# Kernel tuning notes

Measured on AMD Instinct MI355X. Metric: run time of the kernel, lower is better.

Reference implementation:

```python
import jax, jax.numpy as jnp
import numpy as np

B, C, H, W = 8, 256, 128, 128
KC, VC, HEADS = 256, 256, 8


def setup_inputs() -> dict:
    key = jax.random.key(0)
    ks = jax.random.split(key, 10)
    s = 0.05
    return {
        "x": jax.random.normal(ks[0], (B, C, H, W), jnp.float32),
        "Wk": jax.random.normal(ks[1], (KC, C), jnp.float32) * s,
        "bk": jax.random.normal(ks[2], (KC,), jnp.float32) * s,
        "Wq": jax.random.normal(ks[3], (KC, C), jnp.float32) * s,
        "bq": jax.random.normal(ks[4], (KC,), jnp.float32) * s,
        "Wv": jax.random.normal(ks[5], (VC, C), jnp.float32) * s,
        "bv": jax.random.normal(ks[6], (VC,), jnp.float32) * s,
        "Wr": jax.random.normal(ks[7], (C, VC), jnp.float32) * s,
        "br": jax.random.normal(ks[8], (C,), jnp.float32) * s,
        "head_count": HEADS,
    }


def reference(x, Wk, bk, Wq, bq, Wv, bv, Wr, br, head_count):
    n, c, h, w = x.shape
    hw = h * w
    xf = x.reshape(n, c, hw)  # [n, C, S]
    # 1x1 convs == per-pixel linear projections
    keys = jnp.einsum('kc,ncs->nks', Wk, xf) + bk[None, :, None]
    queries = jnp.einsum('kc,ncs->nks', Wq, xf) + bq[None, :, None]
    values = jnp.einsum('vc,ncs->nvs', Wv, xf) + bv[None, :, None]

    dk = Wk.shape[0] // head_count
    dv = Wv.shape[0] // head_count
    # split heads along channel dim (matches torch channel slicing)
    K = jax.nn.softmax(keys.reshape(n, head_count, dk, hw), axis=-1)   # softmax over spatial
    Q = jax.nn.softmax(queries.reshape(n, head_count, dk, hw), axis=2) # softmax over key dim
    V = values.reshape(n, head_count, dv, hw)

    # context = K @ V^T : [n, h, dk, dv]
    ctx = jnp.einsum('nhks,nhvs->nhkv', K, V)
    # attended = ctx^T @ Q : [n, h, dv, S]
    att = jnp.einsum('nhkv,nhks->nhvs', ctx, Q).reshape(n, head_count * dv, h, w)

    attention = jnp.einsum('ov,nvhw->nohw', Wr, att) + br[None, :, None, None]
    # attention map: per-head mean over key dim, then mean over heads
    attention_map = K.mean(axis=2).mean(axis=1).reshape(n, h, w)
    # torch returns the LAST head's context (loop variable after the loop)
    context_last = ctx[:, -1]
    return attention, context_last, attention_map
```

## Files before the change

kernel.cpp:

```cpp
#include <hip/hip_runtime.h>
#include <hip/hip_bf16.h>

typedef float f32x4 __attribute__((ext_vector_type(4)));
typedef short s16x8 __attribute__((ext_vector_type(8)));
typedef short s16x4 __attribute__((ext_vector_type(4)));
typedef __bf16 bf16x8 __attribute__((ext_vector_type(8)));
typedef unsigned short u16;

#define DEVI __device__ __forceinline__

static constexpr int    HW      = 16384;
static constexpr size_t BSTRIDE = (size_t)256 * HW;

static constexpr size_t oXBT   = 0;
static constexpr size_t oEK    = oXBT  + (size_t)8 * HW * 256 * 2;
static constexpr size_t oQT    = oEK   + (size_t)8 * 256 * HW * 2;
static constexpr size_t oVB    = oQT   + (size_t)8 * HW * 256 * 2;
static constexpr size_t oWK    = oVB   + (size_t)8 * 256 * HW * 2;
static constexpr size_t oBIAS  = oWK   + (size_t)768 * 256 * 2;
static constexpr size_t oISE   = oBIAS + 4096;
static constexpr size_t oPS    = oISE  + 8192;
static constexpr size_t oCTX   = oPS   + (size_t)256 * 2048 * 4;
static constexpr size_t oMB    = oCTX  + (size_t)64 * 1024 * 4;
static constexpr size_t oCPART = oMB   + (size_t)8 * 256 * 256 * 2;
static constexpr size_t oMPART = oCPART + (size_t)4096 * 1024 * 4;

DEVI float bf2f(short x) {
  unsigned u = ((unsigned)(unsigned short)x) << 16;
  return __builtin_bit_cast(float, u);
}
DEVI u16 f2bf(float x) { return __builtin_bit_cast(u16, (__bf16)x); }

DEVI void gld16(const void* g, void* l) {
  __builtin_amdgcn_global_load_lds(
      (__attribute__((address_space(1))) void*)(g),
      (__attribute__((address_space(3))) void*)(l), 16, 0, 0);
}

__global__ __launch_bounds__(256) void k_pt(
    const float* __restrict__ x,
    const float* __restrict__ Wk, const float* __restrict__ Wq, const float* __restrict__ Wv,
    const float* __restrict__ bk, const float* __restrict__ bq, const float* __restrict__ bv,
    u16* __restrict__ xbT, u16* __restrict__ Wkqv, float* __restrict__ bias)
{
  __shared__ u16 lds[64 * 256];
  const int t = threadIdx.x;
  const int tb = blockIdx.x;
  if (tb < 2048) {
    const int n = tb >> 8;
    const int s0 = (tb & 255) * 64;
    const float* src = x + ((size_t)n * 256 + t) * HW + s0;
    #pragma unroll
    for (int i = 0; i < 16; ++i) {
      f32x4 v = *(const f32x4*)(src + i * 4);
      #pragma unroll
      for (int j = 0; j < 4; ++j) lds[(i * 4 + j) * 256 + t] = f2bf(v[j]);
    }
    __syncthreads();
    s16x8* gp = (s16x8*)(xbT + (size_t)n * BSTRIDE + (size_t)s0 * 256);
    const s16x8* lp = (const s16x8*)lds;
    #pragma unroll
    for (int i = 0; i < 8; ++i) gp[t + i * 256] = lp[t + i * 256];
  } else {
    const int i = (tb - 2048) * 256 + t;
    for (int p = i; p < 768 * 256; p += 64 * 256) {
      float v = (p < 65536) ? Wk[p] : (p < 131072 ? Wq[p - 65536] : Wv[p - 131072]);
      Wkqv[p] = f2bf(v);
    }
    if (i < 768) bias[i] = (i < 256) ? bk[i] : (i < 512 ? bq[i - 256] : bv[i - 512]);
  }
}

#define GEMM_CORE(Ab, Bb)                                                                   \
  u16* Al = smem;                                                                           \
  u16* Bl = smem + 16384;                                                                   \
  auto STAGE = [&](int buf, int kt) {                                                       \
    const int k0 = kt * 64;                                                                 \
    _Pragma("unroll")                                                                       \
    for (int i = 0; i < 4; ++i) {                                                           \
      const int r_ = i * 32 + (t >> 3);                                                     \
      const int cs = (((t & 7) ^ (r_ & 7)) * 8);                                            \
      gld16((Ab) + (size_t)r_ * 256 + k0 + cs, Al + buf * 8192 + i * 2048 + t * 8);         \
      gld16((Bb) + (size_t)r_ * 256 + k0 + cs, Bl + buf * 8192 + i * 2048 + t * 8);         \
    }                                                                                       \
  };                                                                                        \
  f32x4 acc[4][4] = {};                                                                     \
  STAGE(0, 0); STAGE(1, 1);                                                                 \
  _Pragma("unroll")                                                                         \
  for (int kt = 0; kt < 4; ++kt) {                                                          \
    if (kt < 3) asm volatile("s_waitcnt vmcnt(8)" ::: "memory");                            \
    else        asm volatile("s_waitcnt vmcnt(0)" ::: "memory");                            \
    __builtin_amdgcn_s_barrier();                                                           \
    const int buf = kt & 1;                                                                 \
    _Pragma("unroll")                                                                       \
    for (int ks = 0; ks < 2; ++ks) {                                                        \
      bf16x8 af[4], bff[4];                                                                 \
      _Pragma("unroll")                                                                     \
      for (int g = 0; g < 4; ++g) {                                                         \
        const int mrow = wm + g * 16 + l15;                                                 \
        const int srow = wn + g * 16 + l15;                                                 \
        af[g]  = *(const bf16x8*)&Al[buf * 8192 + mrow * 64 + (((ks * 4 + l4) ^ (mrow & 7)) * 8)]; \
        bff[g] = *(const bf16x8*)&Bl[buf * 8192 + srow * 64 + (((ks * 4 + l4) ^ (srow & 7)) * 8)]; \
      }                                                                                     \
      __builtin_amdgcn_s_setprio(1);                                                        \
      _Pragma("unroll")                                                                     \
      for (int mg = 0; mg < 4; ++mg)                                                        \
        _Pragma("unroll")                                                                   \
        for (int ng = 0; ng < 4; ++ng)                                                      \
          acc[mg][ng] = __builtin_amdgcn_mfma_f32_16x16x32_bf16(af[mg], bff[ng], acc[mg][ng], 0, 0, 0); \
      __builtin_amdgcn_s_setprio(0);                                                        \
    }                                                                                       \
    asm volatile("s_waitcnt lgkmcnt(0)" ::: "memory");                                      \
    __builtin_amdgcn_s_barrier();                                                           \
    if (kt < 2) STAGE(buf, kt + 2);                                                         \
  }

__global__ __launch_bounds__(256, 2) void k_proj(
    const u16* __restrict__ W, const u16* __restrict__ xbT, const float* __restrict__ bias,
    u16* __restrict__ ek, u16* __restrict__ qT, u16* __restrict__ vb, float* __restrict__ ps)
{
  __shared__ u16 smem[32768];
  const int t = threadIdx.x;
  const int L = blockIdx.x;
  const int n = L & 7;
  const int idx = L >> 3;
  const int lane = t & 63;
  const int l15 = lane & 15, l4 = (lane >> 4) & 3;
  const int wv = t >> 6;
  const int wm = (wv & 1) * 64, wn = (wv >> 1) * 64;

  if (idx < 128) {
    const int mbi = idx & 3;
    const int sq  = idx >> 2;
    const bool isK = (mbi < 2);
    const int m0 = (mbi & 1) * 128;
    const int aBase = (isK ? 0 : 512) + m0;
    const u16* Ab = W + (size_t)aBase * 256;
    const u16* Bb = xbT + (size_t)n * BSTRIDE;
    u16* Al = smem;
    u16* Bl = smem + 16384;

    float biasv[4];
    #pragma unroll
    for (int mf = 0; mf < 4; ++mf) biasv[mf] = bias[aBase + wm + mf * 16 + l15];

    const int rr = t >> 3;
    const int csh = t & 7;
    auto STAGE = [&](int buf, int it) {
      const int k0 = (it & 3) * 64;
      const size_t s_t0 = (size_t)((sq * 4 + (it >> 2)) * 128);
      #pragma unroll
      for (int i = 0; i < 4; ++i) {
        const int row = i * 32 + rr;
        const int cs = (csh ^ (row & 7)) * 8;
        gld16(Ab + (size_t)row * 256 + k0 + cs,  Al + buf * 8192 + i * 2048 + t * 8);
        gld16(Bb + (s_t0 + row) * 256 + k0 + cs, Bl + buf * 8192 + i * 2048 + t * 8);
      }
    };

    f32x4 acc[4][4] = {};
    STAGE(0, 0); STAGE(1, 1);
    u16* outb = (isK ? ek : vb) + (size_t)n * BSTRIDE;

    #pragma unroll
    for (int it = 0; it < 16; ++it) {
      if (it == 15)                          asm volatile("s_waitcnt vmcnt(0)" ::: "memory");
      else if ((it & 3) <= 1 && it >= 4) {
        if (isK) asm volatile("s_waitcnt vmcnt(28)" ::: "memory");
        else     asm volatile("s_waitcnt vmcnt(24)" ::: "memory");
      } else                                 asm volatile("s_waitcnt vmcnt(8)" ::: "memory");
      __builtin_amdgcn_s_barrier();

      const int buf = it & 1;
      #pragma unroll
      for (int ks = 0; ks < 2; ++ks) {
        bf16x8 af[4], bff[4];
        #pragma unroll
        for (int g = 0; g < 4; ++g) {
          const int mrow = wm + g * 16 + l15;
          const int srow = wn + g * 16 + l15;
          af[g]  = *(const bf16x8*)&Al[buf * 8192 + mrow * 64 + (((ks * 4 + l4) ^ (mrow & 7)) * 8)];
          bff[g] = *(const bf16x8*)&Bl[buf * 8192 + srow * 64 + (((ks * 4 + l4) ^ (srow & 7)) * 8)];
        }
        __builtin_amdgcn_s_setprio(1);
        #pragma unroll
        for (int sf = 0; sf < 4; ++sf)
          #pragma unroll
          for (int mf = 0; mf < 4; ++mf)
            acc[sf][mf] = __builtin_amdgcn_mfma_f32_16x16x32_bf16(bff[sf], af[mf], acc[sf][mf], 0, 0, 0);
        __builtin_amdgcn_s_setprio(0);
      }
      asm volatile("s_waitcnt lgkmcnt(0)" ::: "memory");
      __builtin_amdgcn_s_barrier();
      if (it < 14) STAGE(buf, it + 2);

      if ((it & 3) == 3) {
        const int tile = it >> 2;
        const int s0t = (sq * 4 + tile) * 128;
        const int stile = sq * 4 + tile;
        if (isK) {
          float rs[4] = {0.f, 0.f, 0.f, 0.f};
          #pragma unroll
          for (int sf = 0; sf < 4; ++sf)
            #pragma unroll
            for (int mf = 0; mf < 4; ++mf) {
              s16x4 pk;
              #pragma unroll
              for (int r = 0; r < 4; ++r) {
                const float e = __expf(acc[sf][mf][r] + biasv[mf]);
                rs[mf] += e;
                pk[r] = (short)f2bf(e);
              }
              *(s16x4*)(outb + (size_t)(m0 + wm + mf * 16 + l15) * HW + s0t + wn + sf * 16 + l4 * 4) = pk;
            }
          #pragma unroll
          for (int mf = 0; mf < 4; ++mf) {
            float v = rs[mf];
            v += __shfl_xor(v, 16); v += __shfl_xor(v, 32);
            if (l4 == 0)
              ps[((size_t)(stile * 2 + (wn >> 6))) * 2048 + n * 256 + m0 + wm + mf * 16 + l15] = v;
          }
        } else {
          #pragma unroll
          for (int sf = 0; sf < 4; ++sf)
            #pragma unroll
            for (int mf = 0; mf < 4; ++mf) {
              s16x4 pk;
              #pragma unroll
              for (int r = 0; r < 4; ++r) pk[r] = (short)f2bf(acc[sf][mf][r] + biasv[mf]);
              *(s16x4*)(outb + (size_t)(m0 + wm + mf * 16 + l15) * HW + s0t + wn + sf * 16 + l4 * 4) = pk;
            }
        }
        #pragma unroll
        for (int sf = 0; sf < 4; ++sf)
          #pragma unroll
          for (int mf = 0; mf < 4; ++mf) acc[sf][mf] = f32x4{0.f, 0.f, 0.f, 0.f};
      }
    }
  } else {
    const int qidx = idx - 128;
    const int mbq = qidx & 1;
    const int sb  = qidx >> 1;
    const int m0 = 256 + mbq * 128, s0 = sb * 128;
    const u16* Ab = W + (size_t)m0 * 256;
    const u16* Bb = xbT + (size_t)n * BSTRIDE + (size_t)s0 * 256;

    GEMM_CORE(Ab, Bb)

    #pragma unroll
    for (int mg = 0; mg < 4; ++mg)
      #pragma unroll
      for (int r = 0; r < 4; ++r) {
        const float bb = bias[m0 + wm + mg * 16 + l4 * 4 + r];
        #pragma unroll
        for (int ng = 0; ng < 4; ++ng) acc[mg][ng][r] += bb;
      }

    #pragma unroll
    for (int hh = 0; hh < 2; ++hh)
      #pragma unroll
      for (int ng = 0; ng < 4; ++ng) {
        float s = 0.f;
        #pragma unroll
        for (int mg = hh * 2; mg < hh * 2 + 2; ++mg)
          #pragma unroll
          for (int r = 0; r < 4; ++r) { const float e = __expf(acc[mg][ng][r]); acc[mg][ng][r] = e; s += e; }
        s += __shfl_xor(s, 16);
        s += __shfl_xor(s, 32);
        const float inv = 1.f / s;
        #pragma unroll
        for (int mg = hh * 2; mg < hh * 2 + 2; ++mg)
          #pragma unroll
          for (int r = 0; r < 4; ++r) acc[mg][ng][r] *= inv;
      }
    __syncthreads();
    #pragma unroll
    for (int mg = 0; mg < 4; ++mg)
      #pragma unroll
      for (int ng = 0; ng < 4; ++ng)
        #pragma unroll
        for (int r = 0; r < 4; ++r) {
          const int srow = wn + ng * 16 + l15;
          const int mcol = wm + mg * 16 + l4 * 4 + r;
          smem[srow * 136 + mcol] = f2bf(acc[mg][ng][r]);
        }
    __syncthreads();
    u16* O = qT + (size_t)n * BSTRIDE + (size_t)s0 * 256 + mbq * 128;
    #pragma unroll
    for (int it = 0; it < 8; ++it) {
      const int row = it * 16 + (t >> 4);
      *(s16x8*)(O + (size_t)row * 256 + (t & 15) * 8) = *(const s16x8*)&smem[row * 136 + (t & 15) * 8];
    }
  }
}

__global__ __launch_bounds__(256) void k_inv(const float* __restrict__ ps, float* __restrict__ ise)
{
  const int i = blockIdx.x * 256 + threadIdx.x;
  float s = 0.f;
  for (int b = 0; b < 256; ++b) s += ps[(size_t)b * 2048 + i];
  ise[i] = 1.f / s;
}

__global__ __launch_bounds__(64) void k_ctx_part(
    const u16* __restrict__ ek, const u16* __restrict__ vb, const float* __restrict__ ise,
    float* __restrict__ cpart, float* __restrict__ mpart)
{
  const int blk = blockIdx.x;
  const int chunk = blk & 63, nh = blk >> 6;
  const int h = nh & 7, n = nh >> 3;
  const int lane = threadIdx.x;
  const int l15 = lane & 15, l4 = lane >> 4;
  const u16* kb = ek + ((size_t)n * 256 + h * 32) * HW;
  const u16* vv = vb + ((size_t)n * 256 + h * 32) * HW;
  const float iv0 = ise[n * 256 + h * 32 + l15];
  const float iv1 = ise[n * 256 + h * 32 + 16 + l15];
  f32x4 acc[2][2] = {};
  float macc[8][8] = {};
  const int sbase = chunk * 256 + l4 * 8;
  #pragma unroll
  for (int ks = 0; ks < 8; ++ks) {
    const int sb = sbase + ks * 32;
    bf16x8 ef[2], vf[2];
    #pragma unroll
    for (int g = 0; g < 2; ++g) {
      ef[g] = *(const bf16x8*)(kb + (size_t)(g * 16 + l15) * HW + sb);
      vf[g] = *(const bf16x8*)(vv + (size_t)(g * 16 + l15) * HW + sb);
    }
    #pragma unroll
    for (int j = 0; j < 8; ++j)
      macc[ks][j] = fmaf(iv0, (float)ef[0][j], fmaf(iv1, (float)ef[1][j], macc[ks][j]));
    #pragma unroll
    for (int a = 0; a < 2; ++a)
      #pragma unroll
      for (int b = 0; b < 2; ++b)
        acc[a][b] = __builtin_amdgcn_mfma_f32_16x16x32_bf16(ef[a], vf[b], acc[a][b], 0, 0, 0);
  }
  float* op = cpart + (size_t)blk * 1024;
  #pragma unroll
  for (int a = 0; a < 2; ++a)
    #pragma unroll
    for (int b = 0; b < 2; ++b)
      #pragma unroll
      for (int r = 0; r < 4; ++r)
        op[(a * 16 + l4 * 4 + r) * 32 + b * 16 + l15] = acc[a][b][r];
  #pragma unroll
  for (int ks = 0; ks < 8; ++ks)
    #pragma unroll
    for (int j = 0; j < 8; ++j) {
      float v = macc[ks][j];
      v += __shfl_xor(v, 1); v += __shfl_xor(v, 2);
      v += __shfl_xor(v, 4); v += __shfl_xor(v, 8);
      macc[ks][j] = v;
    }
  if (l15 == 0) {
    float* mp = mpart + ((size_t)h * 8 + n) * HW + sbase;
    #pragma unroll
    for (int ks = 0; ks < 8; ++ks) {
      f32x4 a = {macc[ks][0], macc[ks][1], macc[ks][2], macc[ks][3]};
      f32x4 b = {macc[ks][4], macc[ks][5], macc[ks][6], macc[ks][7]};
      *(f32x4*)(mp + ks * 32)     = a;
      *(f32x4*)(mp + ks * 32 + 4) = b;
    }
  }
}

__global__ __launch_bounds__(256) void k_post(
    const float* __restrict__ cpart, const float* __restrict__ ise,
    const float* __restrict__ Wr, const float* __restrict__ mpart,
    u16* __restrict__ Mb, float* __restrict__ dctx, float* __restrict__ dmap)
{
  const int t = threadIdx.x;
  if (blockIdx.x < 64) {
    const int nh = blockIdx.x, n = nh >> 3, h = nh & 7;
    __shared__ float cl[1024];
    f32x4 a = {};
    for (int c = 0; c < 64; ++c) a += *(const f32x4*)(cpart + ((size_t)nh * 64 + c) * 1024 + t * 4);
    const float inv = ise[n * 256 + h * 32 + (t >> 3)];
    a *= inv;
    *(f32x4*)(cl + t * 4) = a;
    if (h == 7) *(f32x4*)(dctx + (size_t)n * 1024 + t * 4) = a;
    __syncthreads();
    const int o = t;
    float wr[32];
    const float* wp = Wr + (size_t)o * 256 + h * 32;
    #pragma unroll
    for (int v = 0; v < 32; ++v) wr[v] = wp[v];
    u16* mp = Mb + ((size_t)n * 256 + o) * 256 + h * 32;
    #pragma unroll 4
    for (int k = 0; k < 32; ++k) {
      float s = 0.f;
      #pragma unroll
      for (int v = 0; v < 32; ++v) s += wr[v] * cl[k * 32 + v];
      mp[k] = f2bf(s);
    }
  } else {
    const int i = (blockIdx.x - 64) * 256 + t;
    f32x4 a = {};
    #pragma unroll
    for (int h = 0; h < 8; ++h) a += *(const f32x4*)(mpart + (size_t)h * 131072 + (size_t)i * 4);
    a *= (1.0f / 256.0f);
    *(f32x4*)(dmap + (size_t)i * 4) = a;
  }
}

__global__ __launch_bounds__(256, 2) void k_attn2(
    const u16* __restrict__ Mb, const u16* __restrict__ qT, const float* __restrict__ br,
    float* __restrict__ Out)
{
  __shared__ u16 smem[32768];
  const int t = threadIdx.x;
  const int L = blockIdx.x;
  const int n = L & 7;
  const int idx = L >> 3;
  const int mb = idx & 1;
  const int sq = idx >> 1;
  const int m0 = mb * 128;
  const int lane = t & 63;
  const int l15 = lane & 15, l4 = (lane >> 4) & 3;
  const int wv = t >> 6;
  const int wm = (wv & 1) * 64, wn = (wv >> 1) * 64;
  const u16* Ab = Mb + (size_t)n * 65536 + (size_t)m0 * 256;
  const u16* Bb = qT + (size_t)n * BSTRIDE;
  u16* Al = smem;
  u16* Bl = smem + 16384;

  float biasv[4];
  #pragma unroll
  for (int mf = 0; mf < 4; ++mf) biasv[mf] = br[m0 + wm + mf * 16 + l15];

  const int rr = t >> 3;
  const int csh = t & 7;
  auto STAGE = [&](int buf, int it) {
    const int k0 = (it & 3) * 64;
    const size_t s_t0 = (size_t)((sq * 4 + (it >> 2)) * 128);
    #pragma unroll
    for (int i = 0; i < 4; ++i) {
      const int row = i * 32 + rr;
      const int cs = (csh ^ (row & 7)) * 8;
      gld16(Ab + (size_t)row * 256 + k0 + cs,  Al + buf * 8192 + i * 2048 + t * 8);
      gld16(Bb + (s_t0 + row) * 256 + k0 + cs, Bl + buf * 8192 + i * 2048 + t * 8);
    }
  };

  f32x4 acc[4][4] = {};
  STAGE(0, 0); STAGE(1, 1);

  float* ob = Out + (size_t)n * BSTRIDE;

  #pragma unroll
  for (int it = 0; it < 16; ++it) {
    if (it == 15)                          asm volatile("s_waitcnt vmcnt(0)" ::: "memory");
    else if ((it & 3) <= 1 && it >= 4)     asm volatile("s_waitcnt vmcnt(24)" ::: "memory");
    else                                   asm volatile("s_waitcnt vmcnt(8)" ::: "memory");
    __builtin_amdgcn_s_barrier();

    const int buf = it & 1;
    #pragma unroll
    for (int ks = 0; ks < 2; ++ks) {
      bf16x8 af[4], bff[4];
      #pragma unroll
      for (int g = 0; g < 4; ++g) {
        const int mrow = wm + g * 16 + l15;
        const int srow = wn + g * 16 + l15;
        af[g]  = *(const bf16x8*)&Al[buf * 8192 + mrow * 64 + (((ks * 4 + l4) ^ (mrow & 7)) * 8)];
        bff[g] = *(const bf16x8*)&Bl[buf * 8192 + srow * 64 + (((ks * 4 + l4) ^ (srow & 7)) * 8)];
      }
      __builtin_amdgcn_s_setprio(1);
      #pragma unroll
      for (int sf = 0; sf < 4; ++sf)
        #pragma unroll
        for (int mf = 0; mf < 4; ++mf)
          acc[sf][mf] = __builtin_amdgcn_mfma_f32_16x16x32_bf16(bff[sf], af[mf], acc[sf][mf], 0, 0, 0);
      __builtin_amdgcn_s_setprio(0);
    }
    asm volatile("s_waitcnt lgkmcnt(0)" ::: "memory");
    __builtin_amdgcn_s_barrier();
    if (it < 14) STAGE(buf, it + 2);

    if ((it & 3) == 3) {
      const int s0t = (sq * 4 + (it >> 2)) * 128;
      #pragma unroll
      for (int sf = 0; sf < 4; ++sf)
        #pragma unroll
        for (int mf = 0; mf < 4; ++mf) {
          f32x4 o = acc[sf][mf] + biasv[mf];
          *(f32x4*)(ob + (size_t)(m0 + wm + mf * 16 + l15) * HW + s0t + wn + sf * 16 + l4 * 4) = o;
          acc[sf][mf] = f32x4{0.f, 0.f, 0.f, 0.f};
        }
    }
  }
}

extern "C" void kernel_launch(void* const* d_in, const int* in_sizes, int n_in,
                              void* d_out, int out_size, void* d_ws, size_t ws_size,
                              hipStream_t stream)
{
  (void)in_sizes; (void)n_in; (void)out_size; (void)ws_size;
  const float* x  = (const float*)d_in[0];
  const float* Wk = (const float*)d_in[1];
  const float* bk = (const float*)d_in[2];
  const float* Wq = (const float*)d_in[3];
  const float* bq = (const float*)d_in[4];
  const float* Wv = (const float*)d_in[5];
  const float* bv = (const float*)d_in[6];
  const float* Wr = (const float*)d_in[7];
  const float* br = (const float*)d_in[8];

  char* ws = (char*)d_ws;
  u16*   xbT  = (u16*)(ws + oXBT);
  u16*   ek   = (u16*)(ws + oEK);
  u16*   qT   = (u16*)(ws + oQT);
  u16*   vb   = (u16*)(ws + oVB);
  u16*   Wkqv = (u16*)(ws + oWK);
  float* bias = (float*)(ws + oBIAS);
  float* ise  = (float*)(ws + oISE);
  float* ps   = (float*)(ws + oPS);
  u16*   Mb   = (u16*)(ws + oMB);
  float* cpart= (float*)(ws + oCPART);
  float* mpart= (float*)(ws + oMPART);

  float* attn = (float*)d_out;
  float* dctx = (float*)d_out + 33554432;
  float* dmap = (float*)d_out + 33562624;

  k_pt<<<2112, 256, 0, stream>>>(x, Wk, Wq, Wv, bk, bq, bv, xbT, Wkqv, bias);
  k_proj<<<3072, 256, 0, stream>>>(Wkqv, xbT, bias, ek, qT, vb, ps);
  k_inv<<<8, 256, 0, stream>>>(ps, ise);
  k_ctx_part<<<4096, 64, 0, stream>>>(ek, vb, ise, cpart, mpart);
  k_post<<<192, 256, 0, stream>>>(cpart, ise, Wr, mpart, Mb, dctx, dmap);
  k_attn2<<<512, 256, 0, stream>>>(Mb, qT, br, attn);
}
```

Measured before the change: 283.8 us.

## Fuse K, V and Q projections per spatial tile with resident x tile in LDS

Restructures the projection kernel so each block loads a 128x256 tile of the transposed input once into LDS and reuses it for the K, V and Q projections of one 128-channel half. Only the weight slices are streamed, double-buffered in 32-wide k steps. The old scheme had separate blocks for K/V and Q that each re-read the x tiles. This cuts global x traffic and the grid size, at the cost of more LDS per block (80KB), which may lower occupancy, and more barriers from the smaller k steps.

```diff
diff --git a/kernel.cpp b/kernel.cpp
--- a/kernel.cpp
+++ b/kernel.cpp
@@ -71,226 +71,181 @@
   }
 }
 
-#define GEMM_CORE(Ab, Bb)                                                                   \
-  u16* Al = smem;                                                                           \
-  u16* Bl = smem + 16384;                                                                   \
-  auto STAGE = [&](int buf, int kt) {                                                       \
-    const int k0 = kt * 64;                                                                 \
-    _Pragma("unroll")                                                                       \
-    for (int i = 0; i < 4; ++i) {                                                           \
-      const int r_ = i * 32 + (t >> 3);                                                     \
-      const int cs = (((t & 7) ^ (r_ & 7)) * 8);                                            \
-      gld16((Ab) + (size_t)r_ * 256 + k0 + cs, Al + buf * 8192 + i * 2048 + t * 8);         \
-      gld16((Bb) + (size_t)r_ * 256 + k0 + cs, Bl + buf * 8192 + i * 2048 + t * 8);         \
-    }                                                                                       \
-  };                                                                                        \
-  f32x4 acc[4][4] = {};                                                                     \
-  STAGE(0, 0); STAGE(1, 1);                                                                 \
-  _Pragma("unroll")                                                                         \
-  for (int kt = 0; kt < 4; ++kt) {                                                          \
-    if (kt < 3) asm volatile("s_waitcnt vmcnt(8)" ::: "memory");                            \
-    else        asm volatile("s_waitcnt vmcnt(0)" ::: "memory");                            \
-    __builtin_amdgcn_s_barrier();                                                           \
-    const int buf = kt & 1;                                                                 \
-    _Pragma("unroll")                                                                       \
-    for (int ks = 0; ks < 2; ++ks) {                                                        \
-      bf16x8 af[4], bff[4];                                                                 \
-      _Pragma("unroll")                                                                     \
-      for (int g = 0; g < 4; ++g) {                                                         \
-        const int mrow = wm + g * 16 + l15;                                                 \
-        const int srow = wn + g * 16 + l15;                                                 \
-        af[g]  = *(const bf16x8*)&Al[buf * 8192 + mrow * 64 + (((ks * 4 + l4) ^ (mrow & 7)) * 8)]; \
-        bff[g] = *(const bf16x8*)&Bl[buf * 8192 + srow * 64 + (((ks * 4 + l4) ^ (srow & 7)) * 8)]; \
-      }                                                                                     \
-      __builtin_amdgcn_s_setprio(1);                                                        \
-      _Pragma("unroll")                                                                     \
-      for (int mg = 0; mg < 4; ++mg)                                                        \
-        _Pragma("unroll")                                                                   \
-        for (int ng = 0; ng < 4; ++ng)                                                      \
-          acc[mg][ng] = __builtin_amdgcn_mfma_f32_16x16x32_bf16(af[mg], bff[ng], acc[mg][ng], 0, 0, 0); \
-      __builtin_amdgcn_s_setprio(0);                                                        \
-    }                                                                                       \
-    asm volatile("s_waitcnt lgkmcnt(0)" ::: "memory");                                      \
-    __builtin_amdgcn_s_barrier();                                                           \
-    if (kt < 2) STAGE(buf, kt + 2);                                                         \
-  }
-
-__global__ __launch_bounds__(256, 2) void k_proj(
+__global__ __launch_bounds__(256, 2) void k_proj3(
     const u16* __restrict__ W, const u16* __restrict__ xbT, const float* __restrict__ bias,
     u16* __restrict__ ek, u16* __restrict__ qT, u16* __restrict__ vb, float* __restrict__ ps)
 {
-  __shared__ u16 smem[32768];
+  __shared__ u16 smem[40960];
   const int t = threadIdx.x;
   const int L = blockIdx.x;
   const int n = L & 7;
   const int idx = L >> 3;
+  const int mh = idx & 1;
+  const int sb = idx >> 1;
+  const int m0 = mh * 128;
+  const int s0 = sb * 128;
   const int lane = t & 63;
   const int l15 = lane & 15, l4 = (lane >> 4) & 3;
   const int wv = t >> 6;
   const int wm = (wv & 1) * 64, wn = (wv >> 1) * 64;
 
-  if (idx < 128) {
-    const int mbi = idx & 3;
-    const int sq  = idx >> 2;
-    const bool isK = (mbi < 2);
-    const int m0 = (mbi & 1) * 128;
-    const int aBase = (isK ? 0 : 512) + m0;
-    const u16* Ab = W + (size_t)aBase * 256;
-    const u16* Bb = xbT + (size_t)n * BSTRIDE;
-    u16* Al = smem;
-    u16* Bl = smem + 16384;
-
-    float biasv[4];
-    #pragma unroll
-    for (int mf = 0; mf < 4; ++mf) biasv[mf] = bias[aBase + wm + mf * 16 + l15];
-
-    const int rr = t >> 3;
-    const int csh = t & 7;
-    auto STAGE = [&](int buf, int it) {
-      const int k0 = (it & 3) * 64;
-      const size_t s_t0 = (size_t)((sq * 4 + (it >> 2)) * 128);
-      #pragma unroll
-      for (int i = 0; i < 4; ++i) {
-        const int row = i * 32 + rr;
-        const int cs = (csh ^ (row & 7)) * 8;
-        gld16(Ab + (size_t)row * 256 + k0 + cs,  Al + buf * 8192 + i * 2048 + t * 8);
-        gld16(Bb + (s_t0 + row) * 256 + k0 + cs, Bl + buf * 8192 + i * 2048 + t * 8);
+  const u16* Bb = xbT + (size_t)n * BSTRIDE + (size_t)s0 * 256;
+
+  float bK[4], bV[4];
+  #pragma unroll
+  for (int mf = 0; mf < 4; ++mf) {
+    bK[mf] = bias[m0 + wm + mf * 16 + l15];
+    bV[mf] = bias[512 + m0 + wm + mf * 16 + l15];
+  }
+
+  #pragma unroll
+  for (int i = 0; i < 16; ++i) {
+    const int f = i * 256 + t;
+    const int row = f >> 5, c = f & 31;
+    gld16(Bb + (size_t)row * 256 + ((c ^ (row & 7)) * 8), smem + f * 8);
+  }
+
+  auto STAGEA = [&](int g) {
+    const int kt = g & 7;
+    const int op = g >> 3;
+    const int wr0 = (op == 0) ? 0 : (op == 1 ? 512 : 256);
+    const u16* Ab = W + (size_t)(wr0 + m0) * 256;
+    #pragma unroll
+    for (int i = 0; i < 2; ++i) {
+      const int f = i * 256 + t;
+      const int row = f >> 2, c = f & 3;
+      gld16(Ab + (size_t)row * 256 + kt * 32 + ((c ^ (row & 3)) * 8),
+            smem + 32768 + (g & 1) * 4096 + f * 8);
+    }
+  };
+
+  STAGEA(0); STAGEA(1);
+
+  f32x4 acc[4][4] = {};
+  u16* ekb = ek + (size_t)n * BSTRIDE;
+  u16* vbb = vb + (size_t)n * BSTRIDE;
+
+  #pragma unroll
+  for (int g = 0; g < 24; ++g) {
+    if (g == 23) asm volatile("s_waitcnt vmcnt(0)" ::: "memory");
+    else         asm volatile("s_waitcnt vmcnt(2)" ::: "memory");
+    __builtin_amdgcn_s_barrier();
+
+    const int kt = g & 7;
+    bf16x8 af[4], bff[4];
+    #pragma unroll
+    for (int gg = 0; gg < 4; ++gg) {
+      const int mrow = wm + gg * 16 + l15;
+      const int srow = wn + gg * 16 + l15;
+      const int cidx = kt * 4 + l4;
+      af[gg]  = *(const bf16x8*)&smem[32768 + (g & 1) * 4096 + mrow * 32 + ((l4 ^ (mrow & 3)) * 8)];
+      bff[gg] = *(const bf16x8*)&smem[srow * 256 + ((cidx ^ (srow & 7)) * 8)];
+    }
+    __builtin_amdgcn_s_setprio(1);
+    if (g < 16) {
+      #pragma unroll
+      for (int sf = 0; sf < 4; ++sf)
+        #pragma unroll
+        for (int mf = 0; mf < 4; ++mf)
+          acc[sf][mf] = __builtin_amdgcn_mfma_f32_16x16x32_bf16(bff[sf], af[mf], acc[sf][mf], 0, 0, 0);
+    } else {
+      #pragma unroll
+      for (int mg = 0; mg < 4; ++mg)
+        #pragma unroll
+        for (int ng = 0; ng < 4; ++ng)
+          acc[mg][ng] = __builtin_amdgcn_mfma_f32_16x16x32_bf16(af[mg], bff[ng], acc[mg][ng], 0, 0, 0);
+    }
+    __builtin_amdgcn_s_setprio(0);
+
+    asm volatile("s_waitcnt lgkmcnt(0)" ::: "memory");
+    __builtin_amdgcn_s_barrier();
+    if (g < 22) STAGEA(g + 2);
+
+    if (g == 7) {
+      float rs[4] = {0.f, 0.f, 0.f, 0.f};
+      #pragma unroll
+      for (int sf = 0; sf < 4; ++sf)
+        #pragma unroll
+        for (int mf = 0; mf < 4; ++mf) {
+          s16x4 pk;
+          #pragma unroll
+          for (int r = 0; r < 4; ++r) {
+            const float e = __expf(acc[sf][mf][r] + bK[mf]);
+            rs[mf] += e;
+            pk[r] = (short)f2bf(e);
+          }
+          *(s16x4*)(ekb + (size_t)(m0 + wm + mf * 16 + l15) * HW + s0 + wn + sf * 16 + l4 * 4) = pk;
+        }
+      #pragma unroll
+      for (int mf = 0; mf < 4; ++mf) {
+        float v = rs[mf];
+        v += __shfl_xor(v, 16); v += __shfl_xor(v, 32);
+        if (l4 == 0)
+          ps[((size_t)(sb * 2 + (wn >> 6))) * 2048 + n * 256 + m0 + wm + mf * 16 + l15] = v;
       }
-    };
-
-    f32x4 acc[4][4] = {};
-    STAGE(0, 0); STAGE(1, 1);
-    u16* outb = (isK ? ek : vb) + (size_t)n * BSTRIDE;
-
-    #pragma unroll
-    for (int it = 0; it < 16; ++it) {
-      if (it == 15)                          asm volatile("s_waitcnt vmcnt(0)" ::: "memory");
-      else if ((it & 3) <= 1 && it >= 4) {
-        if (isK) asm volatile("s_waitcnt vmcnt(28)" ::: "memory");
-        else     asm volatile("s_waitcnt vmcnt(24)" ::: "memory");
-      } else                                 asm volatile("s_waitcnt vmcnt(8)" ::: "memory");
-      __builtin_amdgcn_s_barrier();
-
-      const int buf = it & 1;
-      #pragma unroll
-      for (int ks = 0; ks < 2; ++ks) {
-        bf16x8 af[4], bff[4];
-        #pragma unroll
-        for (int g = 0; g < 4; ++g) {
-          const int mrow = wm + g * 16 + l15;
-          const int srow = wn + g * 16 + l15;
-          af[g]  = *(const bf16x8*)&Al[buf * 8192 + mrow * 64 + (((ks * 4 + l4) ^ (mrow & 7)) * 8)];
-          bff[g] = *(const bf16x8*)&Bl[buf * 8192 + srow * 64 + (((ks * 4 + l4) ^ (srow & 7)) * 8)];
+      #pragma unroll
+      for (int sf = 0; sf < 4; ++sf)
+        #pragma unroll
+        for (int mf = 0; mf < 4; ++mf) acc[sf][mf] = f32x4{0.f, 0.f, 0.f, 0.f};
+    } else if (g == 15) {
+      #pragma unroll
+      for (int sf = 0; sf < 4; ++sf)
+        #pragma unroll
+        for (int mf = 0; mf < 4; ++mf) {
+          s16x4 pk;
+          #pragma unroll
+          for (int r = 0; r < 4; ++r) pk[r] = (short)f2bf(acc[sf][mf][r] + bV[mf]);
+          *(s16x4*)(vbb + (size_t)(m0 + wm + mf * 16 + l15) * HW + s0 + wn + sf * 16 + l4 * 4) = pk;
         }
-        __builtin_amdgcn_s_setprio(1);
-        #pragma unroll
-        for (int sf = 0; sf < 4; ++sf)
-          #pragma unroll
-          for (int mf = 0; mf < 4; ++mf)
-            acc[sf][mf] = __builtin_amdgcn_mfma_f32_16x16x32_bf16(bff[sf], af[mf], acc[sf][mf], 0, 0, 0);
-        __builtin_amdgcn_s_setprio(0);
+      #pragma unroll
+      for (int sf = 0; sf < 4; ++sf)
+        #pragma unroll
+        for (int mf = 0; mf < 4; ++mf) acc[sf][mf] = f32x4{0.f, 0.f, 0.f, 0.f};
+    }
+  }
+
+  #pragma unroll
+  for (int mg = 0; mg < 4; ++mg)
+    #pragma unroll
+    for (int r = 0; r < 4; ++r) {
+      const float bb = bias[256 + m0 + wm + mg * 16 + l4 * 4 + r];
+      #pragma unroll
+      for (int ng = 0; ng < 4; ++ng) acc[mg][ng][r] += bb;
+    }
+  #pragma unroll
+  for (int hh = 0; hh < 2; ++hh)
+    #pragma unroll
+    for (int ng = 0; ng < 4; ++ng) {
+      float s = 0.f;
+      #pragma unroll
+      for (int mg = hh * 2; mg < hh * 2 + 2; ++mg)
+        #pragma unroll
+        for (int r = 0; r < 4; ++r) { const float e = __expf(acc[mg][ng][r]); acc[mg][ng][r] = e; s += e; }
+      s += __shfl_xor(s, 16);
+      s += __shfl_xor(s, 32);
+      const float inv = 1.f / s;
+      #pragma unroll
+      for (int mg = hh * 2; mg < hh * 2 + 2; ++mg)
+        #pragma unroll
+        for (int r = 0; r < 4; ++r) acc[mg][ng][r] *= inv;
+    }
+  __syncthreads();
+  #pragma unroll
+  for (int mg = 0; mg < 4; ++mg)
+    #pragma unroll
+    for (int ng = 0; ng < 4; ++ng)
+      #pragma unroll
+      for (int r = 0; r < 4; ++r) {
+        const int srow = wn + ng * 16 + l15;
+        const int mcol = wm + mg * 16 + l4 * 4 + r;
+        smem[srow * 136 + mcol] = f2bf(acc[mg][ng][r]);
       }
-      asm volatile("s_waitcnt lgkmcnt(0)" ::: "memory");
-      __builtin_amdgcn_s_barrier();
-      if (it < 14) STAGE(buf, it + 2);
-
-      if ((it & 3) == 3) {
-        const int tile = it >> 2;
-        const int s0t = (sq * 4 + tile) * 128;
-        const int stile = sq * 4 + tile;
-        if (isK) {
-          float rs[4] = {0.f, 0.f, 0.f, 0.f};
-          #pragma unroll
-          for (int sf = 0; sf < 4; ++sf)
-            #pragma unroll
-            for (int mf = 0; mf < 4; ++mf) {
-              s16x4 pk;
-              #pragma unroll
-              for (int r = 0; r < 4; ++r) {
-                const float e = __expf(acc[sf][mf][r] + biasv[mf]);
-                rs[mf] += e;
-                pk[r] = (short)f2bf(e);
-              }
-              *(s16x4*)(outb + (size_t)(m0 + wm + mf * 16 + l15) * HW + s0t + wn + sf * 16 + l4 * 4) = pk;
-            }
-          #pragma unroll
-          for (int mf = 0; mf < 4; ++mf) {
-            float v = rs[mf];
-            v += __shfl_xor(v, 16); v += __shfl_xor(v, 32);
-            if (l4 == 0)
-              ps[((size_t)(stile * 2 + (wn >> 6))) * 2048 + n * 256 + m0 + wm + mf * 16 + l15] = v;
-          }
-        } else {
-          #pragma unroll
-          for (int sf = 0; sf < 4; ++sf)
-            #pragma unroll
-            for (int mf = 0; mf < 4; ++mf) {
-              s16x4 pk;
-              #pragma unroll
-              for (int r = 0; r < 4; ++r) pk[r] = (short)f2bf(acc[sf][mf][r] + biasv[mf]);
-              *(s16x4*)(outb + (size_t)(m0 + wm + mf * 16 + l15) * HW + s0t + wn + sf * 16 + l4 * 4) = pk;
-            }
-        }
-        #pragma unroll
-        for (int sf = 0; sf < 4; ++sf)
-          #pragma unroll
-          for (int mf = 0; mf < 4; ++mf) acc[sf][mf] = f32x4{0.f, 0.f, 0.f, 0.f};
-      }
-    }
-  } else {
-    const int qidx = idx - 128;
-    const int mbq = qidx & 1;
-    const int sb  = qidx >> 1;
-    const int m0 = 256 + mbq * 128, s0 = sb * 128;
-    const u16* Ab = W + (size_t)m0 * 256;
-    const u16* Bb = xbT + (size_t)n * BSTRIDE + (size_t)s0 * 256;
-
-    GEMM_CORE(Ab, Bb)
-
-    #pragma unroll
-    for (int mg = 0; mg < 4; ++mg)
-      #pragma unroll
-      for (int r = 0; r < 4; ++r) {
-        const float bb = bias[m0 + wm + mg * 16 + l4 * 4 + r];
-        #pragma unroll
-        for (int ng = 0; ng < 4; ++ng) acc[mg][ng][r] += bb;
-      }
-
-    #pragma unroll
-    for (int hh = 0; hh < 2; ++hh)
-      #pragma unroll
-      for (int ng = 0; ng < 4; ++ng) {
-        float s = 0.f;
-        #pragma unroll
-        for (int mg = hh * 2; mg < hh * 2 + 2; ++mg)
-          #pragma unroll
-          for (int r = 0; r < 4; ++r) { const float e = __expf(acc[mg][ng][r]); acc[mg][ng][r] = e; s += e; }
-        s += __shfl_xor(s, 16);
-        s += __shfl_xor(s, 32);
-        const float inv = 1.f / s;
-        #pragma unroll
-        for (int mg = hh * 2; mg < hh * 2 + 2; ++mg)
-          #pragma unroll
-          for (int r = 0; r < 4; ++r) acc[mg][ng][r] *= inv;
-      }
-    __syncthreads();
-    #pragma unroll
-    for (int mg = 0; mg < 4; ++mg)
-      #pragma unroll
-      for (int ng = 0; ng < 4; ++ng)
-        #pragma unroll
-        for (int r = 0; r < 4; ++r) {
-          const int srow = wn + ng * 16 + l15;
-          const int mcol = wm + mg * 16 + l4 * 4 + r;
-          smem[srow * 136 + mcol] = f2bf(acc[mg][ng][r]);
-        }
-    __syncthreads();
-    u16* O = qT + (size_t)n * BSTRIDE + (size_t)s0 * 256 + mbq * 128;
-    #pragma unroll
-    for (int it = 0; it < 8; ++it) {
-      const int row = it * 16 + (t >> 4);
-      *(s16x8*)(O + (size_t)row * 256 + (t & 15) * 8) = *(const s16x8*)&smem[row * 136 + (t & 15) * 8];
-    }
+  __syncthreads();
+  u16* O = qT + (size_t)n * BSTRIDE + (size_t)s0 * 256 + mh * 128;
+  #pragma unroll
+  for (int it = 0; it < 8; ++it) {
+    const int row = it * 16 + (t >> 4);
+    *(s16x8*)(O + (size_t)row * 256 + (t & 15) * 8) = *(const s16x8*)&smem[row * 136 + (t & 15) * 8];
   }
 }
 
@@ -525,7 +480,7 @@
   float* dmap = (float*)d_out + 33562624;
 
   k_pt<<<2112, 256, 0, stream>>>(x, Wk, Wq, Wv, bk, bq, bv, xbT, Wkqv, bias);
-  k_proj<<<3072, 256, 0, stream>>>(Wkqv, xbT, bias, ek, qT, vb, ps);
+  k_proj3<<<2048, 256, 0, stream>>>(Wkqv, xbT, bias, ek, qT, vb, ps);
   k_inv<<<8, 256, 0, stream>>>(ps, ise);
   k_ctx_part<<<4096, 64, 0, stream>>>(ek, vb, ise, cpart, mpart);
   k_post<<<192, 256, 0, stream>>>(cpart, ise, Wr, mpart, Mb, dctx, dmap);
```

Result: faster. 274.3 us (-3.4%).
